# Optimization experiments

Measured on AMD Instinct MI355X. Metric: run time of the kernel, lower is better.

## Reference

```python
import jax, jax.numpy as jnp
import numpy as np

HIDDEN = 1024
HEADS = 16
HEAD_DIM = HIDDEN // HEADS
EPS = 1e-6


def _layernorm(x, gamma, beta):
    mu = jnp.mean(x, axis=-1, keepdims=True)
    var = jnp.mean(jnp.square(x - mu), axis=-1, keepdims=True)
    return (x - mu) * jax.lax.rsqrt(var + EPS) * gamma + beta


def setup_inputs() -> dict:
    key = jax.random.key(0)
    ks = jax.random.split(key, 16)
    B, S, D = 2, 2048, HIDDEN
    s = 1.0 / np.sqrt(D)
    inp = {
        "x": jax.random.normal(ks[0], (B, S, D), dtype=jnp.float32),
        "Wq": jax.random.uniform(ks[1], (D, D), jnp.float32, -s, s),
        "bq": jnp.zeros((D,), jnp.float32),
        "Wk": jax.random.uniform(ks[2], (D, D), jnp.float32, -s, s),
        "bk": jnp.zeros((D,), jnp.float32),
        "Wv": jax.random.uniform(ks[3], (D, D), jnp.float32, -s, s),
        "bv": jnp.zeros((D,), jnp.float32),
        "Wo": jax.random.uniform(ks[4], (D, D), jnp.float32, -s, s),
        "bo": jnp.zeros((D,), jnp.float32),
        "g1": jnp.ones((D,), jnp.float32),
        "b1": jnp.zeros((D,), jnp.float32),
        "Wup": jax.random.uniform(ks[5], (D, 4 * D), jnp.float32, -s, s),
        "bup": jnp.zeros((4 * D,), jnp.float32),
        "Wdn": jax.random.uniform(ks[6], (4 * D, D), jnp.float32, -0.5 * s, 0.5 * s),
        "bdn": jnp.zeros((D,), jnp.float32),
        "g2": jnp.ones((D,), jnp.float32),
        "b2": jnp.zeros((D,), jnp.float32),
    }
    return inp


def _forward(x, Wq, bq, Wk, bk, Wv, bv, Wo, bo, g1, b1, Wup, bup, Wdn, bdn, g2, b2):
    B, S, D = x.shape
    H, Hd = HEADS, HEAD_DIM
    # projections -> (B, H, S, Hd)
    q = (x @ Wq + bq).reshape(B, S, H, Hd).transpose(0, 2, 1, 3)
    k = (x @ Wk + bk).reshape(B, S, H, Hd).transpose(0, 2, 1, 3)
    v = (x @ Wv + bv).reshape(B, S, H, Hd).transpose(0, 2, 1, 3)
    # full NxN scores (faithful to the source: explicit QK^T, mask, softmax, AV)
    scores = jnp.einsum("bhqd,bhkd->bhqk", q, k) / np.sqrt(Hd)
    causal = jnp.tril(jnp.ones((S, S), dtype=bool))  # (S, S)
    scores = jnp.where(causal, scores, jnp.float32(-1e20))
    attn = jax.nn.softmax(scores, axis=-1)
    # dropout is identity in eval mode
    mid = jnp.einsum("bhqk,bhkd->bqhd", attn, v).reshape(B, S, D)
    attn_out = mid @ Wo + bo
    x = _layernorm(x + attn_out, g1, b1)
    # FFN
    up = jax.nn.relu(x @ Wup + bup)
    down = up @ Wdn + bdn
    return _layernorm(x + down, g2, b2)


def reference(x, Wq, bq, Wk, bk, Wv, bv, Wo, bo, g1, b1, Wup, bup, Wdn, bdn, g2, b2):
    return _forward(x, Wq, bq, Wk, bk, Wv, bv, Wo, bo, g1, b1, Wup, bup, Wdn, bdn, g2, b2)
```

## Files before the change

kernel.cpp:

```cpp
#include <hip/hip_runtime.h>

#define D_MODEL 1024
#define D_FFN   4096
#define SEQ     2048
#define NROWS   4096
#define QKV_LD  3072
#define BKG     64

typedef __bf16 bf16x8 __attribute__((ext_vector_type(8)));
typedef float  floatx4 __attribute__((ext_vector_type(4)));

__device__ __forceinline__ unsigned short f2bf(float f) {
  unsigned int u = __float_as_uint(f);
  u += 0x7FFFu + ((u >> 16) & 1u);
  return (unsigned short)(u >> 16);
}

template <int C>
__device__ __forceinline__ float ror16(float x) {
  return __int_as_float(
      __builtin_amdgcn_mov_dpp(__float_as_int(x), 0x120 | C, 0xf, 0xf, true));
}

__device__ __forceinline__ void async16(const unsigned short* g, unsigned short* l) {
  __builtin_amdgcn_global_load_lds(
      (const __attribute__((address_space(1))) unsigned int*)g,
      (__attribute__((address_space(3))) unsigned int*)l, 16, 0, 0);
}

__global__ __launch_bounds__(256) void k_f32_to_bf16(
    const float* __restrict__ in, unsigned short* __restrict__ outp, long n) {
  long i = ((long)blockIdx.x * 256 + threadIdx.x) * 4;
  if (i >= n) return;
  float4 v = *(const float4*)(in + i);
  ushort4 o;
  o.x = f2bf(v.x); o.y = f2bf(v.y); o.z = f2bf(v.z); o.w = f2bf(v.w);
  *(ushort4*)(outp + i) = o;
}

__global__ __launch_bounds__(256) void k_transpose_bf16(
    const float* __restrict__ W, unsigned short* __restrict__ WT, int R, int C) {
  __shared__ float tile[32][33];
  int tx = threadIdx.x & 31, ty = threadIdx.x >> 5;
  long bx = (long)blockIdx.x * 32;
  long by = (long)blockIdx.y * 32;
  #pragma unroll
  for (int j = 0; j < 4; j++)
    tile[ty + j * 8][tx] = W[(by + ty + j * 8) * C + bx + tx];
  __syncthreads();
  #pragma unroll
  for (int j = 0; j < 4; j++)
    WT[(bx + ty + j * 8) * R + by + tx] = f2bf(tile[tx][ty + j * 8]);
}

__global__ __launch_bounds__(256) void k_transpose_sq(
    const float* __restrict__ Wq, const float* __restrict__ Wk,
    const float* __restrict__ Wv, const float* __restrict__ Wo,
    unsigned short* __restrict__ WqkvT, unsigned short* __restrict__ WoT) {
  __shared__ float tile[32][33];
  int z = blockIdx.z;
  const float* W = (z == 0) ? Wq : (z == 1) ? Wk : (z == 2) ? Wv : Wo;
  unsigned short* dst = (z < 3) ? (WqkvT + (size_t)z * D_MODEL * D_MODEL) : WoT;
  int tx = threadIdx.x & 31, ty = threadIdx.x >> 5;
  long bx = (long)blockIdx.x * 32;
  long by = (long)blockIdx.y * 32;
  #pragma unroll
  for (int j = 0; j < 4; j++)
    tile[ty + j * 8][tx] = W[(by + ty + j * 8) * D_MODEL + bx + tx];
  __syncthreads();
  #pragma unroll
  for (int j = 0; j < 4; j++)
    dst[(bx + ty + j * 8) * D_MODEL + by + tx] = f2bf(tile[tx][ty + j * 8]);
}

__global__ __launch_bounds__(256) void k_pack_bias(
    const float* __restrict__ bq, const float* __restrict__ bk,
    const float* __restrict__ bv, float* __restrict__ dst) {
  int i = blockIdx.x * 256 + threadIdx.x;
  if (i >= 3072) return;
  float v = (i < 1024) ? bq[i] : (i < 2048) ? bk[i - 1024] : bv[i - 2048];
  dst[i] = v;
}

__global__ __launch_bounds__(256) void k_transpose_v(
    const unsigned short* __restrict__ QKV, unsigned short* __restrict__ Vt) {
  __shared__ unsigned short tile[64][72];
  int r0 = blockIdx.x * 64;
  int c0 = blockIdx.y * 64;
  int tx = threadIdx.x & 15, ty = threadIdx.x >> 4;
  #pragma unroll
  for (int j = 0; j < 4; j++) {
    int r = ty + j * 16;
    *(ushort4*)&tile[r][tx * 4] =
        *(const ushort4*)(QKV + (long)(r0 + r) * QKV_LD + 2048 + c0 + tx * 4);
  }
  __syncthreads();
  #pragma unroll
  for (int j = 0; j < 4; j++) {
    int d = ty + j * 16;
    ushort4 o;
    o.x = tile[tx * 4 + 0][d];
    o.y = tile[tx * 4 + 1][d];
    o.z = tile[tx * 4 + 2][d];
    o.w = tile[tx * 4 + 3][d];
    *(ushort4*)(Vt + (long)(c0 + d) * NROWS + r0 + tx * 4) = o;
  }
}

__global__ __launch_bounds__(256) void k_gemm(
    const unsigned short* __restrict__ A,
    const unsigned short* __restrict__ Bt,
    const float* __restrict__ bias,
    void* __restrict__ Cp, int M, int N, int K, int flags) {
  __shared__ unsigned short As[128 * BKG];
  __shared__ unsigned short Bs[128 * BKG];
  int tid = threadIdx.x, lane = tid & 63, wave = tid >> 6;
  int quad = lane >> 4, l16 = lane & 15;
  int wm = (wave & 1) * 64, wn = (wave >> 1) * 64;
  long bm = (long)blockIdx.x * 128;
  long bn = (long)blockIdx.y * 128;
  int nz = gridDim.z, z = blockIdx.z;
  int Ks = K / nz;
  long zb = (long)z * Ks;

  const floatx4 fz = {0.f, 0.f, 0.f, 0.f};
  floatx4 acc[4][4];
  #pragma unroll
  for (int i = 0; i < 4; i++)
    #pragma unroll
    for (int j = 0; j < 4; j++) acc[i][j] = fz;

  int srow = lane >> 3;
  int sc = (lane & 7) ^ srow;
  const unsigned short* Ag = A + (bm + wave * 8 + srow) * (long)K + zb + sc * 8;
  const unsigned short* Bg = Bt + (bn + wave * 8 + srow) * (long)K + zb + sc * 8;
  unsigned short* Asw = As + wave * 8 * BKG;
  unsigned short* Bsw = Bs + wave * 8 * BKG;

  for (int k0 = 0; k0 < Ks; k0 += BKG) {
    #pragma unroll
    for (int j = 0; j < 4; j++) {
      async16(Ag + (long)j * 32 * K + k0, Asw + j * 32 * BKG);
      async16(Bg + (long)j * 32 * K + k0, Bsw + j * 32 * BKG);
    }
    __syncthreads();
    bf16x8 af[4][2], bfr[4][2];
    #pragma unroll
    for (int i = 0; i < 4; i++) {
      int r = wm + i * 16 + l16;
      int sw = r & 7;
      af[i][0] = *(const bf16x8*)(As + r * BKG + (quad ^ sw) * 8);
      af[i][1] = *(const bf16x8*)(As + r * BKG + ((4 + quad) ^ sw) * 8);
    }
    #pragma unroll
    for (int j = 0; j < 4; j++) {
      int r = wn + j * 16 + l16;
      int sw = r & 7;
      bfr[j][0] = *(const bf16x8*)(Bs + r * BKG + (quad ^ sw) * 8);
      bfr[j][1] = *(const bf16x8*)(Bs + r * BKG + ((4 + quad) ^ sw) * 8);
    }
    #pragma unroll
    for (int h = 0; h < 2; h++)
      #pragma unroll
      for (int i = 0; i < 4; i++)
        #pragma unroll
        for (int j = 0; j < 4; j++)
          acc[i][j] = __builtin_amdgcn_mfma_f32_16x16x32_bf16(af[i][h], bfr[j][h],
                                                             acc[i][j], 0, 0, 0);
    __syncthreads();
  }

  bool f32out = (flags & 1) != 0;
  bool relu   = (flags & 2) != 0;
  float* outf = (float*)Cp + (size_t)z * M * (size_t)N;
  #pragma unroll
  for (int j = 0; j < 4; j++) {
    long col = bn + wn + j * 16 + l16;
    float bvv = (z == 0) ? bias[col] : 0.0f;
    #pragma unroll
    for (int i = 0; i < 4; i++) {
      long row = bm + wm + i * 16 + quad * 4;
      #pragma unroll
      for (int r = 0; r < 4; r++) {
        float v = acc[i][j][r] + bvv;
        if (relu) v = fmaxf(v, 0.0f);
        if (f32out) outf[(row + r) * (long)N + col] = v;
        else        ((unsigned short*)Cp)[(row + r) * (long)N + col] = f2bf(v);
      }
    }
  }
}

#define PLD 72
__global__ __launch_bounds__(256) void k_attn(
    const unsigned short* __restrict__ QKV,
    const unsigned short* __restrict__ Vt,
    unsigned short* __restrict__ Omat) {
  __shared__ unsigned short Ks[64 * 64];
  __shared__ unsigned short Vs[64 * 64];
  __shared__ unsigned short Ps[4][16 * PLD];
  int tid = threadIdx.x;
  int lane = tid & 63, wave = tid >> 6;
  int quad = lane >> 4, l16 = lane & 15;
  int z = blockIdx.x;
  int bh = z & 31;
  int qp = z >> 5;
  int b = bh >> 4, h = bh & 15;
  long rowbase = (long)b * SEQ;
  int hd0 = h * 64;
  unsigned short* pw = &Ps[wave][0];
  const float SCL = 0.18033688f;
  const floatx4 fz = {0.f, 0.f, 0.f, 0.f};

  int r_in = lane >> 3;
  int cpos = lane & 7;

  bf16x8 ones;
  #pragma unroll
  for (int i = 0; i < 8; i++) ones[i] = (__bf16)1.0f;

  #pragma unroll
  for (int phase = 0; phase < 2; phase++) {
    int qt = phase ? qp : (31 - qp);
    int q0w = qt * 64 + wave * 16;
    int qrow = q0w + quad * 4;
    int ntiles = qt + 1;

    bf16x8 qf0, qf1;
    {
      const unsigned short* qp_ =
          QKV + (rowbase + q0w + l16) * (long)QKV_LD + hd0 + quad * 8;
      qf0 = *(const bf16x8*)(qp_);
      qf1 = *(const bf16x8*)(qp_ + 32);
    }

    floatx4 ao[4], aol;
    #pragma unroll
    for (int t = 0; t < 4; t++) ao[t] = fz;
    aol = fz;
    float m_i[4];
    #pragma unroll
    for (int r = 0; r < 4; r++) m_i[r] = -3.0e38f;

    for (int it = 0; it < ntiles; it++) {
      int kv0 = it << 6;
      #pragma unroll
      for (int jj = 0; jj < 2; jj++) {
        int j = wave * 2 + jj;
        int r = j * 8 + r_in;
        int c = cpos ^ (r & 7);
        const unsigned short* gk =
            QKV + (rowbase + kv0 + r) * (long)QKV_LD + 1024 + hd0 + c * 8;
        async16(gk, Ks + j * 512);
        const unsigned short* gv =
            Vt + (long)(hd0 + r) * NROWS + rowbase + kv0 + c * 8;
        async16(gv, Vs + j * 512);
      }
      __syncthreads();

      floatx4 sacc[4];
      #pragma unroll
      for (int t = 0; t < 4; t++) {
        int row = t * 16 + l16;
        int sw = row & 7;
        bf16x8 kf0 = *(const bf16x8*)(Ks + row * 64 + (quad ^ sw) * 8);
        bf16x8 kf1 = *(const bf16x8*)(Ks + row * 64 + ((quad + 4) ^ sw) * 8);
        sacc[t] = __builtin_amdgcn_mfma_f32_16x16x32_bf16(qf0, kf0, fz, 0, 0, 0);
        sacc[t] = __builtin_amdgcn_mfma_f32_16x16x32_bf16(qf1, kf1, sacc[t], 0, 0, 0);
      }

      bool maskt = (it == ntiles - 1);
      if (maskt) {
        #pragma unroll
        for (int t = 0; t < 4; t++) {
          int kvc = kv0 + t * 16 + l16;
          #pragma unroll
          for (int r = 0; r < 4; r++) {
            float s = sacc[t][r] * SCL;
            sacc[t][r] = (kvc > qrow + r) ? -1.0e30f : s;
          }
        }
      } else {
        #pragma unroll
        for (int t = 0; t < 4; t++)
          #pragma unroll
          for (int r = 0; r < 4; r++) sacc[t][r] *= SCL;
      }

      float Mg = sacc[0][0];
      #pragma unroll
      for (int t = 0; t < 4; t++)
        #pragma unroll
        for (int r = 0; r < 4; r++) Mg = fmaxf(Mg, sacc[t][r]);
      Mg = fmaxf(Mg, ror16<1>(Mg));
      Mg = fmaxf(Mg, ror16<2>(Mg));
      Mg = fmaxf(Mg, ror16<4>(Mg));
      Mg = fmaxf(Mg, ror16<8>(Mg));

      float alpha[4];
      #pragma unroll
      for (int r = 0; r < 4; r++) {
        float mn = fmaxf(m_i[r], Mg);
        alpha[r] = __builtin_amdgcn_exp2f(m_i[r] - mn);
        m_i[r] = mn;
      }

      #pragma unroll
      for (int t = 0; t < 4; t++)
        #pragma unroll
        for (int r = 0; r < 4; r++) {
          float p = __builtin_amdgcn_exp2f(sacc[t][r] - m_i[r]);
          pw[(quad * 4 + r) * PLD + t * 16 + l16] =
              (unsigned short)(__float_as_uint(p) >> 16);
        }

      #pragma unroll
      for (int t = 0; t < 4; t++)
        #pragma unroll
        for (int r = 0; r < 4; r++) ao[t][r] *= alpha[r];
      #pragma unroll
      for (int r = 0; r < 4; r++) aol[r] *= alpha[r];

      __asm__ volatile("s_waitcnt lgkmcnt(0)" ::: "memory");
      bf16x8 pf0 = *(const bf16x8*)(pw + l16 * PLD + quad * 8);
      bf16x8 pf1 = *(const bf16x8*)(pw + l16 * PLD + 32 + quad * 8);

      #pragma unroll
      for (int t = 0; t < 4; t++) {
        int row = t * 16 + l16;
        int sw = row & 7;
        bf16x8 vf0 = *(const bf16x8*)(Vs + row * 64 + (quad ^ sw) * 8);
        bf16x8 vf1 = *(const bf16x8*)(Vs + row * 64 + ((quad + 4) ^ sw) * 8);
        ao[t] = __builtin_amdgcn_mfma_f32_16x16x32_bf16(pf0, vf0, ao[t], 0, 0, 0);
        ao[t] = __builtin_amdgcn_mfma_f32_16x16x32_bf16(pf1, vf1, ao[t], 0, 0, 0);
      }
      aol = __builtin_amdgcn_mfma_f32_16x16x32_bf16(pf0, ones, aol, 0, 0, 0);
      aol = __builtin_amdgcn_mfma_f32_16x16x32_bf16(pf1, ones, aol, 0, 0, 0);

      __syncthreads();
    }

    float inv[4];
    #pragma unroll
    for (int r = 0; r < 4; r++) inv[r] = 1.0f / aol[r];
    #pragma unroll
    for (int t = 0; t < 4; t++)
      #pragma unroll
      for (int r = 0; r < 4; r++)
        Omat[(rowbase + qrow + r) * (long)D_MODEL + hd0 + t * 16 + l16] =
            f2bf(ao[t][r] * inv[r]);
  }
}

__global__ __launch_bounds__(256) void k_add_ln(
    const float* __restrict__ A, const float* __restrict__ R1,
    const float* __restrict__ R2,
    const float* __restrict__ g, const float* __restrict__ be,
    float* __restrict__ Y, unsigned short* __restrict__ Ybf) {
  __shared__ float sb[4], ssb[4];
  int tid = threadIdx.x;
  long base = (long)blockIdx.x * D_MODEL + tid * 4;
  float4 a  = *(const float4*)(A + base);
  float4 r1 = *(const float4*)(R1 + base);
  float4 r2 = *(const float4*)(R2 + base);
  float v0 = a.x + r1.x + r2.x, v1 = a.y + r1.y + r2.y;
  float v2 = a.z + r1.z + r2.z, v3 = a.w + r1.w + r2.w;
  float s  = v0 + v1 + v2 + v3;
  float ss = v0 * v0 + v1 * v1 + v2 * v2 + v3 * v3;
  #pragma unroll
  for (int o = 32; o >= 1; o >>= 1) {
    s  += __shfl_xor(s, o, 64);
    ss += __shfl_xor(ss, o, 64);
  }
  int wave = tid >> 6;
  if ((tid & 63) == 0) { sb[wave] = s; ssb[wave] = ss; }
  __syncthreads();
  s  = sb[0] + sb[1] + sb[2] + sb[3];
  ss = ssb[0] + ssb[1] + ssb[2] + ssb[3];
  float mu  = s * (1.0f / 1024.0f);
  float var = ss * (1.0f / 1024.0f) - mu * mu;
  float rstd = rsqrtf(var + 1e-6f);
  float4 gv  = *(const float4*)(g + tid * 4);
  float4 bev = *(const float4*)(be + tid * 4);
  float o0 = (v0 - mu) * rstd * gv.x + bev.x;
  float o1 = (v1 - mu) * rstd * gv.y + bev.y;
  float o2 = (v2 - mu) * rstd * gv.z + bev.z;
  float o3 = (v3 - mu) * rstd * gv.w + bev.w;
  if (Y) *(float4*)(Y + base) = make_float4(o0, o1, o2, o3);
  if (Ybf) {
    ushort4 u;
    u.x = f2bf(o0); u.y = f2bf(o1); u.z = f2bf(o2); u.w = f2bf(o3);
    *(ushort4*)(Ybf + base) = u;
  }
}

extern "C" void kernel_launch(void* const* d_in, const int* in_sizes, int n_in,
                              void* d_out, int out_size, void* d_ws, size_t ws_size,
                              hipStream_t stream) {
  (void)in_sizes; (void)n_in; (void)out_size; (void)ws_size;
  const float* x   = (const float*)d_in[0];
  const float* Wq  = (const float*)d_in[1];
  const float* bq  = (const float*)d_in[2];
  const float* Wk  = (const float*)d_in[3];
  const float* bk  = (const float*)d_in[4];
  const float* Wv  = (const float*)d_in[5];
  const float* bv  = (const float*)d_in[6];
  const float* Wo  = (const float*)d_in[7];
  const float* bo  = (const float*)d_in[8];
  const float* g1  = (const float*)d_in[9];
  const float* b1  = (const float*)d_in[10];
  const float* Wup = (const float*)d_in[11];
  const float* bup = (const float*)d_in[12];
  const float* Wdn = (const float*)d_in[13];
  const float* bdn = (const float*)d_in[14];
  const float* g2  = (const float*)d_in[15];
  const float* b2  = (const float*)d_in[16];
  float* out = (float*)d_out;

  char* ws = (char*)d_ws;
  size_t off = 0;
  auto alloc = [&](size_t bytes) {
    char* p = ws + off;
    off = (off + bytes + 255) & ~(size_t)255;
    return p;
  };
  unsigned short* x_bf   = (unsigned short*)alloc((size_t)NROWS * D_MODEL * 2);
  unsigned short* WqkvT  = (unsigned short*)alloc((size_t)QKV_LD * D_MODEL * 2);
  unsigned short* WoT    = (unsigned short*)alloc((size_t)D_MODEL * D_MODEL * 2);
  unsigned short* WupT   = (unsigned short*)alloc((size_t)D_FFN * D_MODEL * 2);
  unsigned short* WdnT   = (unsigned short*)alloc((size_t)D_MODEL * D_FFN * 2);
  float*          bqkv   = (float*)alloc((size_t)QKV_LD * 4);
  unsigned short* qkv_bf = (unsigned short*)alloc((size_t)NROWS * QKV_LD * 2);
  unsigned short* Vt     = (unsigned short*)alloc((size_t)D_MODEL * NROWS * 2);
  unsigned short* mid_bf = (unsigned short*)alloc((size_t)NROWS * D_MODEL * 2);
  float*          x1f    = (float*)alloc((size_t)NROWS * D_MODEL * 4);
  unsigned short* x1bf   = (unsigned short*)alloc((size_t)NROWS * D_MODEL * 2);
  float*          part   = (float*)alloc((size_t)2 * NROWS * D_MODEL * 4);
  unsigned short* h_bf   = (unsigned short*)alloc((size_t)NROWS * D_FFN * 2);
  float*          part1  = part + (size_t)NROWS * D_MODEL;

  k_f32_to_bf16<<<4096, 256, 0, stream>>>(x, x_bf, (long)NROWS * D_MODEL);
  k_transpose_sq<<<dim3(32, 32, 4), 256, 0, stream>>>(Wq, Wk, Wv, Wo, WqkvT, WoT);
  k_transpose_bf16<<<dim3(128, 32), 256, 0, stream>>>(Wup, WupT, D_MODEL, D_FFN);
  k_transpose_bf16<<<dim3(32, 128), 256, 0, stream>>>(Wdn, WdnT, D_FFN, D_MODEL);
  k_pack_bias<<<12, 256, 0, stream>>>(bq, bk, bv, bqkv);

  k_gemm<<<dim3(32, 24), 256, 0, stream>>>(x_bf, WqkvT, bqkv, qkv_bf,
                                           NROWS, QKV_LD, D_MODEL, 0);
  k_transpose_v<<<dim3(64, 16), 256, 0, stream>>>(qkv_bf, Vt);

  k_attn<<<512, 256, 0, stream>>>(qkv_bf, Vt, mid_bf);

  k_gemm<<<dim3(32, 8, 2), 256, 0, stream>>>(mid_bf, WoT, bo, part,
                                             NROWS, D_MODEL, D_MODEL, 1);
  k_add_ln<<<4096, 256, 0, stream>>>(x, part, part1, g1, b1, x1f, x1bf);

  k_gemm<<<dim3(32, 32), 256, 0, stream>>>(x1bf, WupT, bup, h_bf,
                                           NROWS, D_FFN, D_MODEL, 2);
  k_gemm<<<dim3(32, 8, 2), 256, 0, stream>>>(h_bf, WdnT, bdn, part,
                                             NROWS, D_MODEL, D_FFN, 1);
  k_add_ln<<<4096, 256, 0, stream>>>(x1f, part, part1, g2, b2, out, nullptr);
}
```

Baseline: 388.7 us.

## Replace 128x128 GEMM with double-buffered 256x256 tile kernel and 4-way split-K

Replaces the 128x128, 4-wave GEMM with a 256x256, 8-wave kernel. It double-buffers 128KB of dynamic LDS through async global-to-LDS loads and uses explicit vmcnt/lgkmcnt waits, barriers and s_setprio around the MFMA bursts. Workgroup ids are remapped so consecutive blocks share operands in L2. The N=1024 GEMMs move from 2-way to 4-way split-K, and the add+LayerNorm kernel now sums four partial buffers. The aim is more data reuse per tile and load latency hidden behind the MFMAs. In exchange there are fewer workgroups, e.g. 192 for QKV, 256 for Wo and 256 for FFN-up, which may underfill the 256 CUs, plus extra partial-sum traffic.

```diff
diff --git a/kernel.cpp b/kernel.cpp
--- a/kernel.cpp
+++ b/kernel.cpp
@@ -5,10 +5,11 @@
 #define SEQ     2048
 #define NROWS   4096
 #define QKV_LD  3072
-#define BKG     64
 
 typedef __bf16 bf16x8 __attribute__((ext_vector_type(8)));
 typedef float  floatx4 __attribute__((ext_vector_type(4)));
+
+#define MFMA_BF16 __builtin_amdgcn_mfma_f32_16x16x32_bf16
 
 __device__ __forceinline__ unsigned short f2bf(float f) {
   unsigned int u = __float_as_uint(f);
@@ -107,85 +108,130 @@
   }
 }
 
-__global__ __launch_bounds__(256) void k_gemm(
+__global__ __launch_bounds__(512, 2) void k_gemm256(
     const unsigned short* __restrict__ A,
     const unsigned short* __restrict__ Bt,
     const float* __restrict__ bias,
     void* __restrict__ Cp, int M, int N, int K, int flags) {
-  __shared__ unsigned short As[128 * BKG];
-  __shared__ unsigned short Bs[128 * BKG];
+  extern __shared__ unsigned short lds[];
   int tid = threadIdx.x, lane = tid & 63, wave = tid >> 6;
   int quad = lane >> 4, l16 = lane & 15;
-  int wm = (wave & 1) * 64, wn = (wave >> 1) * 64;
-  long bm = (long)blockIdx.x * 128;
-  long bn = (long)blockIdx.y * 128;
-  int nz = gridDim.z, z = blockIdx.z;
-  int Ks = K / nz;
+  int wm = wave >> 2, wn = wave & 3;
+
+  int nwg = gridDim.x * gridDim.y;
+  int orig = blockIdx.y * gridDim.x + blockIdx.x;
+  int wg = (orig & 7) * (nwg >> 3) + (orig >> 3);
+  long bm = (long)(wg & 15) * 256;
+  long bn = (long)(wg >> 4) * 256;
+
+  int z = blockIdx.z;
+  int Ks = K / gridDim.z;
   long zb = (long)z * Ks;
+  int T = Ks / 64;
 
   const floatx4 fz = {0.f, 0.f, 0.f, 0.f};
-  floatx4 acc[4][4];
-  #pragma unroll
-  for (int i = 0; i < 4; i++)
+  floatx4 acc[8][4];
+  #pragma unroll
+  for (int i = 0; i < 8; i++)
     #pragma unroll
     for (int j = 0; j < 4; j++) acc[i][j] = fz;
 
-  int srow = lane >> 3;
-  int sc = (lane & 7) ^ srow;
-  const unsigned short* Ag = A + (bm + wave * 8 + srow) * (long)K + zb + sc * 8;
-  const unsigned short* Bg = Bt + (bn + wave * 8 + srow) * (long)K + zb + sc * 8;
-  unsigned short* Asw = As + wave * 8 * BKG;
-  unsigned short* Bsw = Bs + wave * 8 * BKG;
-
-  for (int k0 = 0; k0 < Ks; k0 += BKG) {
-    #pragma unroll
-    for (int j = 0; j < 4; j++) {
-      async16(Ag + (long)j * 32 * K + k0, Asw + j * 32 * BKG);
-      async16(Bg + (long)j * 32 * K + k0, Bsw + j * 32 * BKG);
+  int srow = tid >> 3;
+  int sc = (tid & 7) ^ (srow & 7);
+  const unsigned short* Ag = A + (bm + srow) * (long)K + zb + sc * 8;
+  const unsigned short* Bg = Bt + (bn + srow) * (long)K + zb + sc * 8;
+
+  auto stage = [&](int tt, int c) {
+    unsigned short* An = lds + c * 32768;
+    unsigned short* Bn = An + 16384;
+    long ko = (long)tt * 64;
+    #pragma unroll
+    for (int i = 0; i < 4; i++) {
+      async16(Ag + (long)i * 64 * K + ko, An + i * 4096 + wave * 512);
+      async16(Bg + (long)i * 64 * K + ko, Bn + i * 4096 + wave * 512);
     }
-    __syncthreads();
-    bf16x8 af[4][2], bfr[4][2];
-    #pragma unroll
-    for (int i = 0; i < 4; i++) {
-      int r = wm + i * 16 + l16;
-      int sw = r & 7;
-      af[i][0] = *(const bf16x8*)(As + r * BKG + (quad ^ sw) * 8);
-      af[i][1] = *(const bf16x8*)(As + r * BKG + ((4 + quad) ^ sw) * 8);
-    }
-    #pragma unroll
-    for (int j = 0; j < 4; j++) {
-      int r = wn + j * 16 + l16;
-      int sw = r & 7;
-      bfr[j][0] = *(const bf16x8*)(Bs + r * BKG + (quad ^ sw) * 8);
-      bfr[j][1] = *(const bf16x8*)(Bs + r * BKG + ((4 + quad) ^ sw) * 8);
-    }
-    #pragma unroll
-    for (int h = 0; h < 2; h++)
-      #pragma unroll
-      for (int i = 0; i < 4; i++)
-        #pragma unroll
-        for (int j = 0; j < 4; j++)
-          acc[i][j] = __builtin_amdgcn_mfma_f32_16x16x32_bf16(af[i][h], bfr[j][h],
-                                                             acc[i][j], 0, 0, 0);
-    __syncthreads();
+  };
+
+  int aoff = (wm * 128 + l16) * 64;
+  int boff = (wn * 64 + l16) * 64;
+  int sw = l16 & 7;
+  int ca0 = (quad ^ sw) * 8;
+  int ca1 = ((4 + quad) ^ sw) * 8;
+
+  stage(0, 0);
+  for (int t = 0; t < T; t++) {
+    int c = t & 1;
+    const unsigned short* Ac = lds + c * 32768;
+    const unsigned short* Bc = Ac + 16384;
+    int tn = (t + 1 < T) ? t + 1 : T - 1;
+    stage(tn, c ^ 1);
+    __asm__ volatile("s_waitcnt vmcnt(8)" ::: "memory");
+    __builtin_amdgcn_s_barrier();
+
+    bf16x8 af[8], b0, b1;
+    #pragma unroll
+    for (int m = 0; m < 8; m++) af[m] = *(const bf16x8*)(Ac + aoff + m * 1024 + ca0);
+    b0 = *(const bf16x8*)(Bc + boff + 0 * 1024 + ca0);
+    b1 = *(const bf16x8*)(Bc + boff + 1 * 1024 + ca0);
+    __asm__ volatile("s_waitcnt lgkmcnt(0)" ::: "memory");
+    __builtin_amdgcn_s_setprio(1);
+    #pragma unroll
+    for (int m = 0; m < 8; m++) acc[m][0] = MFMA_BF16(af[m], b0, acc[m][0], 0, 0, 0);
+    #pragma unroll
+    for (int m = 0; m < 8; m++) acc[m][1] = MFMA_BF16(af[m], b1, acc[m][1], 0, 0, 0);
+    __builtin_amdgcn_s_setprio(0);
+    __builtin_amdgcn_s_barrier();
+    b0 = *(const bf16x8*)(Bc + boff + 2 * 1024 + ca0);
+    b1 = *(const bf16x8*)(Bc + boff + 3 * 1024 + ca0);
+    __asm__ volatile("s_waitcnt lgkmcnt(0)" ::: "memory");
+    __builtin_amdgcn_s_setprio(1);
+    #pragma unroll
+    for (int m = 0; m < 8; m++) acc[m][2] = MFMA_BF16(af[m], b0, acc[m][2], 0, 0, 0);
+    #pragma unroll
+    for (int m = 0; m < 8; m++) acc[m][3] = MFMA_BF16(af[m], b1, acc[m][3], 0, 0, 0);
+    __builtin_amdgcn_s_setprio(0);
+    __builtin_amdgcn_s_barrier();
+    #pragma unroll
+    for (int m = 0; m < 8; m++) af[m] = *(const bf16x8*)(Ac + aoff + m * 1024 + ca1);
+    b0 = *(const bf16x8*)(Bc + boff + 0 * 1024 + ca1);
+    b1 = *(const bf16x8*)(Bc + boff + 1 * 1024 + ca1);
+    __asm__ volatile("s_waitcnt lgkmcnt(0)" ::: "memory");
+    __builtin_amdgcn_s_setprio(1);
+    #pragma unroll
+    for (int m = 0; m < 8; m++) acc[m][0] = MFMA_BF16(af[m], b0, acc[m][0], 0, 0, 0);
+    #pragma unroll
+    for (int m = 0; m < 8; m++) acc[m][1] = MFMA_BF16(af[m], b1, acc[m][1], 0, 0, 0);
+    __builtin_amdgcn_s_setprio(0);
+    __builtin_amdgcn_s_barrier();
+    b0 = *(const bf16x8*)(Bc + boff + 2 * 1024 + ca1);
+    b1 = *(const bf16x8*)(Bc + boff + 3 * 1024 + ca1);
+    __asm__ volatile("s_waitcnt lgkmcnt(0)" ::: "memory");
+    __builtin_amdgcn_s_setprio(1);
+    #pragma unroll
+    for (int m = 0; m < 8; m++) acc[m][2] = MFMA_BF16(af[m], b0, acc[m][2], 0, 0, 0);
+    #pragma unroll
+    for (int m = 0; m < 8; m++) acc[m][3] = MFMA_BF16(af[m], b1, acc[m][3], 0, 0, 0);
+    __builtin_amdgcn_s_setprio(0);
+    __builtin_amdgcn_s_barrier();
   }
 
   bool f32out = (flags & 1) != 0;
   bool relu   = (flags & 2) != 0;
   float* outf = (float*)Cp + (size_t)z * M * (size_t)N;
-  #pragma unroll
-  for (int j = 0; j < 4; j++) {
-    long col = bn + wn + j * 16 + l16;
+  unsigned short* outh = (unsigned short*)Cp;
+  #pragma unroll
+  for (int n = 0; n < 4; n++) {
+    long col = bn + wn * 64 + n * 16 + l16;
     float bvv = (z == 0) ? bias[col] : 0.0f;
     #pragma unroll
-    for (int i = 0; i < 4; i++) {
-      long row = bm + wm + i * 16 + quad * 4;
+    for (int m = 0; m < 8; m++) {
+      long row = bm + wm * 128 + m * 16 + quad * 4;
       #pragma unroll
       for (int r = 0; r < 4; r++) {
-        float v = acc[i][j][r] + bvv;
+        float v = acc[m][n][r] + bvv;
         if (relu) v = fmaxf(v, 0.0f);
         if (f32out) outf[(row + r) * (long)N + col] = v;
-        else        ((unsigned short*)Cp)[(row + r) * (long)N + col] = f2bf(v);
+        else        outh[(row + r) * (long)N + col] = f2bf(v);
       }
     }
   }
@@ -353,18 +399,22 @@
 }
 
 __global__ __launch_bounds__(256) void k_add_ln(
-    const float* __restrict__ A, const float* __restrict__ R1,
-    const float* __restrict__ R2,
+    const float* __restrict__ A, const float* __restrict__ P,
     const float* __restrict__ g, const float* __restrict__ be,
     float* __restrict__ Y, unsigned short* __restrict__ Ybf) {
   __shared__ float sb[4], ssb[4];
+  const long PS = (long)NROWS * D_MODEL;
   int tid = threadIdx.x;
   long base = (long)blockIdx.x * D_MODEL + tid * 4;
   float4 a  = *(const float4*)(A + base);
-  float4 r1 = *(const float4*)(R1 + base);
-  float4 r2 = *(const float4*)(R2 + base);
-  float v0 = a.x + r1.x + r2.x, v1 = a.y + r1.y + r2.y;
-  float v2 = a.z + r1.z + r2.z, v3 = a.w + r1.w + r2.w;
+  float4 p0 = *(const float4*)(P + base);
+  float4 p1 = *(const float4*)(P + PS + base);
+  float4 p2 = *(const float4*)(P + 2 * PS + base);
+  float4 p3 = *(const float4*)(P + 3 * PS + base);
+  float v0 = a.x + p0.x + p1.x + p2.x + p3.x;
+  float v1 = a.y + p0.y + p1.y + p2.y + p3.y;
+  float v2 = a.z + p0.z + p1.z + p2.z + p3.z;
+  float v3 = a.w + p0.w + p1.w + p2.w + p3.w;
   float s  = v0 + v1 + v2 + v3;
   float ss = v0 * v0 + v1 * v1 + v2 * v2 + v3 * v3;
   #pragma unroll
@@ -398,6 +448,12 @@
                               void* d_out, int out_size, void* d_ws, size_t ws_size,
                               hipStream_t stream) {
   (void)in_sizes; (void)n_in; (void)out_size; (void)ws_size;
+  static bool s_attr = false;
+  if (!s_attr) {
+    hipFuncSetAttribute((const void*)k_gemm256,
+                        hipFuncAttributeMaxDynamicSharedMemorySize, 131072);
+    s_attr = true;
+  }
   const float* x   = (const float*)d_in[0];
   const float* Wq  = (const float*)d_in[1];
   const float* bq  = (const float*)d_in[2];
@@ -435,9 +491,8 @@
   unsigned short* mid_bf = (unsigned short*)alloc((size_t)NROWS * D_MODEL * 2);
   float*          x1f    = (float*)alloc((size_t)NROWS * D_MODEL * 4);
   unsigned short* x1bf   = (unsigned short*)alloc((size_t)NROWS * D_MODEL * 2);
-  float*          part   = (float*)alloc((size_t)2 * NROWS * D_MODEL * 4);
+  float*          part   = (float*)alloc((size_t)4 * NROWS * D_MODEL * 4);
   unsigned short* h_bf   = (unsigned short*)alloc((size_t)NROWS * D_FFN * 2);
-  float*          part1  = part + (size_t)NROWS * D_MODEL;
 
   k_f32_to_bf16<<<4096, 256, 0, stream>>>(x, x_bf, (long)NROWS * D_MODEL);
   k_transpose_sq<<<dim3(32, 32, 4), 256, 0, stream>>>(Wq, Wk, Wv, Wo, WqkvT, WoT);
@@ -445,19 +500,19 @@
   k_transpose_bf16<<<dim3(32, 128), 256, 0, stream>>>(Wdn, WdnT, D_FFN, D_MODEL);
   k_pack_bias<<<12, 256, 0, stream>>>(bq, bk, bv, bqkv);
 
-  k_gemm<<<dim3(32, 24), 256, 0, stream>>>(x_bf, WqkvT, bqkv, qkv_bf,
-                                           NROWS, QKV_LD, D_MODEL, 0);
+  k_gemm256<<<dim3(16, 12, 1), 512, 131072, stream>>>(x_bf, WqkvT, bqkv, qkv_bf,
+                                                      NROWS, QKV_LD, D_MODEL, 0);
   k_transpose_v<<<dim3(64, 16), 256, 0, stream>>>(qkv_bf, Vt);
 
   k_attn<<<512, 256, 0, stream>>>(qkv_bf, Vt, mid_bf);
 
-  k_gemm<<<dim3(32, 8, 2), 256, 0, stream>>>(mid_bf, WoT, bo, part,
-                                             NROWS, D_MODEL, D_MODEL, 1);
-  k_add_ln<<<4096, 256, 0, stream>>>(x, part, part1, g1, b1, x1f, x1bf);
-
-  k_gemm<<<dim3(32, 32), 256, 0, stream>>>(x1bf, WupT, bup, h_bf,
-                                           NROWS, D_FFN, D_MODEL, 2);
-  k_gemm<<<dim3(32, 8, 2), 256, 0, stream>>>(h_bf, WdnT, bdn, part,
-                                             NROWS, D_MODEL, D_FFN, 1);
-  k_add_ln<<<4096, 256, 0, stream>>>(x1f, part, part1, g2, b2, out, nullptr);
-}
+  k_gemm256<<<dim3(16, 4, 4), 512, 131072, stream>>>(mid_bf, WoT, bo, part,
+                                                     NROWS, D_MODEL, D_MODEL, 1);
+  k_add_ln<<<4096, 256, 0, stream>>>(x, part, g1, b1, x1f, x1bf);
+
+  k_gemm256<<<dim3(16, 16, 1), 512, 131072, stream>>>(x1bf, WupT, bup, h_bf,
+                                                      NROWS, D_FFN, D_MODEL, 2);
+  k_gemm256<<<dim3(16, 4, 4), 512, 131072, stream>>>(h_bf, WdnT, bdn, part,
+                                                     NROWS, D_MODEL, D_FFN, 1);
+  k_add_ln<<<4096, 256, 0, stream>>>(x1f, part, g2, b2, out, nullptr);
+}
```

Measured after the change: 388.7 us. About the same (+0.0%).
